# Kernel optimization log

Measured on AMD Instinct MI355X. Metric: run time of the kernel, lower is better.

## Reference

```python
import jax, jax.numpy as jnp
import numpy as np
import math

PHI_INV = 2.0 / (1.0 + math.sqrt(5.0))
BATCH, IN_DIM, OUT_DIM = 2048, 512, 128
N_OSC, N_LAYERS, DT, STEPS = 256, 4, 0.1, 10
MU_GATE_FACTOR = 0.5  # module state z=0.5 lies in [MU_1, MU_P) -> gate * 0.5; z < MU_S so no liminal feedback


def setup_inputs() -> dict:
    key = jax.random.key(0)
    ks = jax.random.split(key, 6)
    x = jax.random.normal(ks[0], (BATCH, IN_DIM), jnp.float32)
    W_enc = jax.random.normal(ks[1], (N_OSC, IN_DIM), jnp.float32) / np.sqrt(IN_DIM).astype(np.float32)
    b_enc = jnp.zeros((N_OSC,), jnp.float32)
    K0 = jax.random.normal(ks[2], (N_LAYERS, N_OSC, N_OSC), jnp.float32) * 0.1
    Ks = (K0 + jnp.swapaxes(K0, -1, -2)) / 2  # symmetric init, as in torch
    omegas = jax.random.normal(ks[3], (N_LAYERS, N_OSC), jnp.float32) * 0.1
    K_globals = jnp.full((N_LAYERS,), 0.5, jnp.float32)
    mu_gates = jnp.ones((N_LAYERS,), jnp.float32)
    W_dec = jax.random.normal(ks[4], (OUT_DIM, N_OSC), jnp.float32) / np.sqrt(N_OSC).astype(np.float32)
    b_dec = jnp.zeros((OUT_DIM,), jnp.float32)
    return dict(x=x, W_enc=W_enc, b_enc=b_enc, Ks=Ks, omegas=omegas,
                K_globals=K_globals, mu_gates=mu_gates, W_dec=W_dec, b_dec=b_dec)


def _wrap(t):
    # torch.atan2(sin, cos) phase wrap to (-pi, pi]
    return jnp.arctan2(jnp.sin(t), jnp.cos(t))


def _kuramoto_layer(theta, K, omega, K_global, mu_gate):
    # theta: [B, n]; K: [n, n]
    K_eff = K * (mu_gate * MU_GATE_FACTOR)
    KT = K_eff.T  # so (s @ KT)[b, i] = sum_j K_eff[i, j] * s[b, j]

    def step(th, _):
        s, c = jnp.sin(th), jnp.cos(th)
        # sum_j K[i,j] * sin(th_j - th_i) = cos_i * (K sin)_i - sin_i * (K cos)_i
        coupling_sum = c * (s @ KT) - s * (c @ KT)
        dtheta = omega + (K_global / N_OSC) * coupling_sum
        return _wrap(th + DT * dtheta), None

    theta, _ = jax.lax.scan(step, theta, None, length=STEPS)
    return theta


def reference(x, W_enc, b_enc, Ks, omegas, K_globals, mu_gates, W_dec, b_dec):
    theta = _wrap(x @ W_enc.T + b_enc)  # [B, n]

    def layer(th, params):
        K, om, kg, mg = params
        return _kuramoto_layer(th, K, om, kg, mg), None

    theta, _ = jax.lax.scan(layer, theta, (Ks, omegas, K_globals, mu_gates))
    coherence = jnp.sqrt(jnp.cos(theta).mean(-1) ** 2 + jnp.sin(theta).mean(-1) ** 2)  # [B]
    output = theta @ W_dec.T + b_dec  # [B, out_dim]
    return output, theta, coherence
```

## Files before the change

kernel.cpp:

```cpp
#include <hip/hip_runtime.h>


#define NB 2048
#define NIN 512
#define NOUT 128
#define NOSC 256
#define DTT 0.1f

#define WS_WENC (512*1024)
#define WS_WD   (1024*1024)

typedef _Float16 f16;
typedef _Float16 f16x4 __attribute__((ext_vector_type(4)));
typedef _Float16 f16x8 __attribute__((ext_vector_type(8)));
typedef float f32x4 __attribute__((ext_vector_type(4)));

__device__ __forceinline__ float wrapf(float t) {
    return t - 6.28318530717958648f * rintf(t * 0.159154943091895336f);
}

__global__ __launch_bounds__(256) void helix_prep(
    const float* __restrict__ Ks, const float* __restrict__ Wenc,
    const float* __restrict__ Wdec, char* __restrict__ ws)
{
    const int g = blockIdx.x * 256 + threadIdx.x;
    if (g < 32768) {
        const int ln = g & 63, lg = ln >> 4, lr = ln & 15;
        const int kf = (g >> 6) & 7, nt = (g >> 9) & 15, l = (g >> 13) & 3;
        const float* s = Ks + (((size_t)l * NOSC + nt * 16 + lr) * NOSC + kf * 32 + lg * 8);
        f16x8 o;
        #pragma unroll
        for (int e = 0; e < 8; ++e) o[e] = (f16)s[e];
        *(f16x8*)(ws + (size_t)g * 16) = o;
    } else if (g < 65536) {
        const int q = g - 32768;
        const int ln = q & 63, lg = ln >> 4, lr = ln & 15;
        const int h = (q >> 6) & 1, kf = (q >> 7) & 15, nt = (q >> 11) & 15;
        const float* s = Wenc + ((size_t)(nt * 16 + lr) * NIN + kf * 32 + lg * 8);
        f16x8 o;
        #pragma unroll
        for (int e = 0; e < 8; ++e) {
            float v = s[e];
            f16 hi = (f16)v;
            o[e] = h ? (f16)(v - (float)hi) : hi;
        }
        *(f16x8*)(ws + WS_WENC + (size_t)q * 16) = o;
    } else if (g < 69632) {
        const int q = g - 65536;
        const int ln = q & 63, lg = ln >> 4, lr = ln & 15;
        const int kf = (q >> 6) & 7, nt = (q >> 9) & 7;
        const float* s = Wdec + ((size_t)(nt * 16 + lr) * NOSC + kf * 32 + lg * 8);
        f16x8 o;
        #pragma unroll
        for (int e = 0; e < 8; ++e) o[e] = (f16)s[e];
        *(f16x8*)(ws + WS_WD + (size_t)q * 16) = o;
    }
}

__global__ __launch_bounds__(1024, 4) void helix11(
    const float* __restrict__ x,
    const float* __restrict__ b_enc,
    const float* __restrict__ omegas,
    const float* __restrict__ Kgl,
    const float* __restrict__ mgl,
    const float* __restrict__ b_dec,
    const char* __restrict__ ws,
    float* __restrict__ out)
{
    __shared__ __align__(16) char smem[25600];
    float* th_lds = (float*)(smem + 16384);
    float* cohPS  = (float*)(smem + 24576);
    float* cohPC  = (float*)(smem + 25088);

    const int tid = threadIdx.x;
    const int wv = tid >> 6, ln = tid & 63, lg = ln >> 4, lr = ln & 15;
    const int d  = lr >> 3;
    const int row0 = blockIdx.x * 8;
    const int jb  = 16 * wv + lr;

    float* out_y   = out;
    float* out_th  = out + (size_t)NB * NOUT;
    float* out_coh = out + (size_t)NB * (NOUT + NOSC);

    const int4 zz = make_int4(0, 0, 0, 0);

    float dtccA[4], omL[4];
    #pragma unroll
    for (int l = 0; l < 4; ++l) {
        dtccA[l] = DTT * Kgl[l] * (1.0f / (float)NOSC) * (mgl[l] * 0.5f);
        omL[l]   = DTT * omegas[l * NOSC + jb];
    }

    {
        const int r  = tid >> 7;
        const int j0 = (tid & 127) << 2;
        float4 v = *(const float4*)(x + (size_t)(row0 + r) * NIN + j0);
        float vv[4] = {v.x, v.y, v.z, v.w};
        f16x4 hi, lo;
        #pragma unroll
        for (int e = 0; e < 4; ++e) {
            hi[e] = (f16)vv[e];
            lo[e] = (f16)(vv[e] - (float)hi[e]);
        }
        char* base = smem + (j0 >> 5) * 1024 + ((j0 >> 3) & 3) * 256 + (j0 & 7) * 2;
        *(f16x4*)(base + (2 * r) * 16)     = hi;
        *(f16x4*)(base + (2 * r + 1) * 16) = lo;
    }
    __syncthreads();

    f16x8 Bf[8];
    auto loadK = [&](const int l) {
        const char* kb = ws + (size_t)l * 131072 + (size_t)wv * 8192 + ln * 16;
        #pragma unroll
        for (int kf = 0; kf < 8; ++kf)
            Bf[kf] = *(const f16x8*)(kb + kf * 1024);
    };

    float th[2], sv[2], cv[2];
    {
        f32x4 accH = {0,0,0,0}, accL = {0,0,0,0};
        const char* aBase = smem + lg * 256 + lr * 16;
        const char* wE = ws + WS_WENC + (size_t)wv * 32768 + ln * 16;
        #pragma unroll 4
        for (int kf = 0; kf < 16; ++kf) {
            f16x8 a  = *(const f16x8*)(aBase + kf * 1024);
            f16x8 bh = *(const f16x8*)(wE + kf * 2048);
            f16x8 bl = *(const f16x8*)(wE + kf * 2048 + 1024);
            accH = __builtin_amdgcn_mfma_f32_16x16x32_f16(a, bh, accH, 0, 0, 0);
            accL = __builtin_amdgcn_mfma_f32_16x16x32_f16(a, bl, accL, 0, 0, 0);
        }
        loadK(0);
        const float be = b_enc[jb];
        #pragma unroll
        for (int p = 0; p < 2; ++p) {
            float tval = accH[2*p] + accH[2*p+1] + accL[2*p] + accL[2*p+1] + be;
            th[p] = wrapf(tval);
            __sincosf(th[p], &sv[p], &cv[p]);
        }
    }
    __syncthreads();

    const int rb = lg * 256 + (lr ^ ((lg & 1) << 1)) * 16;
    const int wbase = (jb >> 5) * 1024 + ((jb >> 3) & 3) * 256 + (lr & 7) * 2;
    const int wz0 = wbase + (((4 * lg + 0) ^ (d << 1)) << 4);
    const int wz1 = wbase + (((4 * lg + 1) ^ (d << 1)) << 4);
    const int wz2 = wbase + (((4 * lg + 2) ^ (d << 1)) << 4);
    const int wz3 = wbase + (((4 * lg + 3) ^ (d << 1)) << 4);

    *(f16*)(smem + wz0) = (f16)sv[0];
    *(f16*)(smem + wz1) = (f16)cv[0];
    *(f16*)(smem + wz2) = (f16)sv[1];
    *(f16*)(smem + wz3) = (f16)cv[1];
    __syncthreads();

    auto STEP = [&](const char* Sb, char* Wb, const float om, const float cc) {
        f32x4 acc = {0.f, 0.f, 0.f, 0.f};
        __builtin_amdgcn_s_setprio(1);
        #pragma unroll
        for (int kf = 0; kf < 8; ++kf) {
            f16x8 a = *(const f16x8*)(Sb + kf * 1024 + rb);
            acc = __builtin_amdgcn_mfma_f32_16x16x32_f16(a, Bf[kf], acc, 0, 0, 0);
        }
        #pragma unroll
        for (int p = 0; p < 2; ++p) {
            float diff = fmaf(cv[p], acc[2*p], -(sv[p] * acc[2*p+1]));
            th[p] += fmaf(diff, cc, om);
            __sincosf(th[p], &sv[p], &cv[p]);
        }
        *(f16*)(Wb + wz0) = (f16)sv[0];
        *(f16*)(Wb + wz1) = (f16)cv[0];
        *(f16*)(Wb + wz2) = (f16)sv[1];
        *(f16*)(Wb + wz3) = (f16)cv[1];
        __builtin_amdgcn_s_setprio(0);
        __syncthreads();
    };

    auto runLayer = [&](const float om, const float cc) {
        #pragma unroll 1
        for (int p5 = 0; p5 < 5; ++p5) {
            STEP(smem,        smem + 8192, om, cc);
            STEP(smem + 8192, smem,        om, cc);
        }
    };

    runLayer(omL[0], dtccA[0]);
    loadK(1); runLayer(omL[1], dtccA[1]);
    loadK(2); runLayer(omL[2], dtccA[2]);
    loadK(3); runLayer(omL[3], dtccA[3]);

    {
        const int dbase = (jb >> 5) * 1024 + ((jb >> 3) & 3) * 256 + (lr & 7) * 2;
        #pragma unroll
        for (int p = 0; p < 2; ++p) {
            const float wt = wrapf(th[p]);
            th_lds[(2 * lg + p) * NOSC + jb] = wt;
            *(f16*)(smem + dbase + (2 * lg + p) * 16) = (f16)wt;
        }
    }
    #pragma unroll
    for (int p = 0; p < 2; ++p) {
        float pS = sv[p], pC = cv[p];
        pS += __shfl_xor(pS, 1); pC += __shfl_xor(pC, 1);
        pS += __shfl_xor(pS, 2); pC += __shfl_xor(pC, 2);
        pS += __shfl_xor(pS, 4); pC += __shfl_xor(pC, 4);
        pS += __shfl_xor(pS, 8); pC += __shfl_xor(pC, 8);
        if (lr == 0) {
            cohPS[wv * 8 + 2 * lg + p] = pS;
            cohPC[wv * 8 + 2 * lg + p] = pC;
        }
    }
    __syncthreads();

    if (tid < 8)
        *(int4*)(smem + tid * 1024 + 128) = zz;
    if (tid < 512) {
        float4 v = ((const float4*)th_lds)[tid];
        *(float4*)(out_th + (size_t)row0 * NOSC + tid * 4) = v;
    }
    if (tid < 8) {
        float S = 0.f, C = 0.f;
        #pragma unroll
        for (int w2 = 0; w2 < 16; ++w2) {
            S += cohPS[w2 * 8 + tid];
            C += cohPC[w2 * 8 + tid];
        }
        S *= (1.0f / (float)NOSC);
        C *= (1.0f / (float)NOSC);
        out_coh[row0 + tid] = sqrtf(S * S + C * C);
    }
    __syncthreads();

    if (wv < 8) {
        const int rbD = (lr < 8) ? (lg * 256 + lr * 16) : 128;
        f32x4 aD = {0.f, 0.f, 0.f, 0.f};
        #pragma unroll
        for (int kf = 0; kf < 8; ++kf) {
            f16x8 a  = *(const f16x8*)(smem + kf * 1024 + rbD);
            f16x8 bw = *(const f16x8*)(ws + WS_WD + (size_t)wv * 8192 + kf * 1024 + ln * 16);
            aD = __builtin_amdgcn_mfma_f32_16x16x32_f16(a, bw, aD, 0, 0, 0);
        }
        if (lg < 2) {
            const int col = 16 * wv + lr;
            const float bd = b_dec[col];
            #pragma unroll
            for (int e = 0; e < 4; ++e)
                out_y[(size_t)(row0 + 4 * lg + e) * NOUT + col] = aD[e] + bd;
        }
    }
}

extern "C" void kernel_launch(void* const* d_in, const int* in_sizes, int n_in,
                              void* d_out, int out_size, void* d_ws, size_t ws_size,
                              hipStream_t stream) {
    const float* x     = (const float*)d_in[0];
    const float* W_enc = (const float*)d_in[1];
    const float* b_enc = (const float*)d_in[2];
    const float* Ks    = (const float*)d_in[3];
    const float* omg   = (const float*)d_in[4];
    const float* Kgl   = (const float*)d_in[5];
    const float* mgl   = (const float*)d_in[6];
    const float* W_dec = (const float*)d_in[7];
    const float* b_dec = (const float*)d_in[8];
    char* ws = (char*)d_ws;

    helix_prep<<<272, 256, 0, stream>>>(Ks, W_enc, W_dec, ws);
    helix11<<<NB / 8, 1024, 0, stream>>>(x, b_enc, omg, Kgl, mgl, b_dec, ws, (float*)d_out);
}
```

Baseline: 41.63 us.

## Double-buffer K fragments across layers and relax step barrier to LDS-only wait

Keeps two register sets for the coupling matrix fragments and prefetches the next layer's K during the first step of the current layer. The per-step __syncthreads is replaced with an lgkmcnt wait plus s_barrier, so outstanding global loads are not drained. The MFMA chain is also split into two independent accumulators to shorten the dependency chain. This costs extra VGPRs under a tight 1024-thread launch bound, which could cause spills.

```diff
diff --git a/kernel.cpp b/kernel.cpp
--- a/kernel.cpp
+++ b/kernel.cpp
@@ -57,7 +57,7 @@
     }
 }
 
-__global__ __launch_bounds__(1024, 4) void helix11(
+__global__ __launch_bounds__(1024, 4) void helix12(
     const float* __restrict__ x,
     const float* __restrict__ b_enc,
     const float* __restrict__ omegas,
@@ -108,12 +108,12 @@
     }
     __syncthreads();
 
-    f16x8 Bf[8];
-    auto loadK = [&](const int l) {
+    f16x8 BfA[8], BfB[8];
+    auto loadK = [&](const int l, f16x8 (&B)[8]) {
         const char* kb = ws + (size_t)l * 131072 + (size_t)wv * 8192 + ln * 16;
         #pragma unroll
         for (int kf = 0; kf < 8; ++kf)
-            Bf[kf] = *(const f16x8*)(kb + kf * 1024);
+            B[kf] = *(const f16x8*)(kb + kf * 1024);
     };
 
     float th[2], sv[2], cv[2];
@@ -129,7 +129,7 @@
             accH = __builtin_amdgcn_mfma_f32_16x16x32_f16(a, bh, accH, 0, 0, 0);
             accL = __builtin_amdgcn_mfma_f32_16x16x32_f16(a, bl, accL, 0, 0, 0);
         }
-        loadK(0);
+        loadK(0, BfA);
         const float be = b_enc[jb];
         #pragma unroll
         for (int p = 0; p < 2; ++p) {
@@ -153,14 +153,18 @@
     *(f16*)(smem + wz3) = (f16)cv[1];
     __syncthreads();
 
-    auto STEP = [&](const char* Sb, char* Wb, const float om, const float cc) {
-        f32x4 acc = {0.f, 0.f, 0.f, 0.f};
+    auto STEP = [&](const char* Sb, char* Wb, const f16x8 (&Bc)[8],
+                    const float om, const float cc) {
+        f32x4 accE = {0.f,0.f,0.f,0.f}, accO = {0.f,0.f,0.f,0.f};
         __builtin_amdgcn_s_setprio(1);
         #pragma unroll
-        for (int kf = 0; kf < 8; ++kf) {
-            f16x8 a = *(const f16x8*)(Sb + kf * 1024 + rb);
-            acc = __builtin_amdgcn_mfma_f32_16x16x32_f16(a, Bf[kf], acc, 0, 0, 0);
-        }
+        for (int kf = 0; kf < 8; kf += 2) {
+            f16x8 a0 = *(const f16x8*)(Sb + kf * 1024 + rb);
+            f16x8 a1 = *(const f16x8*)(Sb + (kf + 1) * 1024 + rb);
+            accE = __builtin_amdgcn_mfma_f32_16x16x32_f16(a0, Bc[kf],     accE, 0, 0, 0);
+            accO = __builtin_amdgcn_mfma_f32_16x16x32_f16(a1, Bc[kf + 1], accO, 0, 0, 0);
+        }
+        f32x4 acc = accE + accO;
         #pragma unroll
         for (int p = 0; p < 2; ++p) {
             float diff = fmaf(cv[p], acc[2*p], -(sv[p] * acc[2*p+1]));
@@ -172,21 +176,24 @@
         *(f16*)(Wb + wz2) = (f16)sv[1];
         *(f16*)(Wb + wz3) = (f16)cv[1];
         __builtin_amdgcn_s_setprio(0);
-        __syncthreads();
+        asm volatile("s_waitcnt lgkmcnt(0)" ::: "memory");
+        __builtin_amdgcn_s_barrier();
     };
 
-    auto runLayer = [&](const float om, const float cc) {
+    auto runLayer = [&](const f16x8 (&Bc)[8], f16x8 (&Bn)[8], const int lNext,
+                        const float om, const float cc) {
         #pragma unroll 1
         for (int p5 = 0; p5 < 5; ++p5) {
-            STEP(smem,        smem + 8192, om, cc);
-            STEP(smem + 8192, smem,        om, cc);
+            if (p5 == 0 && lNext >= 0) loadK(lNext, Bn);
+            STEP(smem,        smem + 8192, Bc, om, cc);
+            STEP(smem + 8192, smem,        Bc, om, cc);
         }
     };
 
-    runLayer(omL[0], dtccA[0]);
-    loadK(1); runLayer(omL[1], dtccA[1]);
-    loadK(2); runLayer(omL[2], dtccA[2]);
-    loadK(3); runLayer(omL[3], dtccA[3]);
+    runLayer(BfA, BfB, 1,  omL[0], dtccA[0]);
+    runLayer(BfB, BfA, 2,  omL[1], dtccA[1]);
+    runLayer(BfA, BfB, 3,  omL[2], dtccA[2]);
+    runLayer(BfB, BfA, -1, omL[3], dtccA[3]);
 
     {
         const int dbase = (jb >> 5) * 1024 + ((jb >> 3) & 3) * 256 + (lr & 7) * 2;
@@ -264,5 +271,5 @@
     char* ws = (char*)d_ws;
 
     helix_prep<<<272, 256, 0, stream>>>(Ks, W_enc, W_dec, ws);
-    helix11<<<NB / 8, 1024, 0, stream>>>(x, b_enc, omg, Kgl, mgl, b_dec, ws, (float*)d_out);
-}
+    helix12<<<NB / 8, 1024, 0, stream>>>(x, b_enc, omg, Kgl, mgl, b_dec, ws, (float*)d_out);
+}
```

After: 42.83 us. 2.9% more time.
